# Kernel optimization log

Hardware: AMD Instinct MI355X
Metric: run time of the kernel (lower is better)

## Reference

```python
import jax, jax.numpy as jnp
import numpy as np

E = 8       # n_experts
TOPK = 2    # n_activated_experts


def setup_inputs() -> dict:
    key = jax.random.key(0)
    ks = jax.random.split(key, 5)
    B, T, C, F = 2, 1024, 1024, 2816
    scale = 0.02
    return {
        "x": jax.random.normal(ks[0], (B, T, C), dtype=jnp.float32),
        "Wg": jax.random.normal(ks[1], (C, E), dtype=jnp.float32) * scale,
        "W1": jax.random.normal(ks[2], (E, C, F), dtype=jnp.float32) * scale,
        "W3": jax.random.normal(ks[3], (E, C, F), dtype=jnp.float32) * scale,
        "W2": jax.random.normal(ks[4], (E, F, C), dtype=jnp.float32) * scale,
    }


def reference(x, Wg, W1, W3, W2):
    B, T, C = x.shape
    xt = x.reshape(-1, C)                                  # [N, C], N = B*T
    router = xt @ Wg                                       # [N, E]
    probs, indices = jax.lax.top_k(router, TOPK)           # [N, K] each, descending like torch.topk
    probs = jax.nn.softmax(probs.astype(jnp.float32), axis=1).astype(x.dtype)
    # combine[n, e] = sum_k probs[n, k] * (indices[n, k] == e)
    onehot = (indices[:, :, None] == jnp.arange(E)).astype(x.dtype)  # [N, K, E]
    combine = jnp.einsum("nk,nke->ne", probs, onehot)      # [N, E]
    # SwiGLU experts, computed densely then combined with routing weights
    h1 = jnp.einsum("nc,ecf->enf", xt, W1)                 # [E, N, F]
    h3 = jnp.einsum("nc,ecf->enf", xt, W3)                 # [E, N, F]
    h = jax.nn.silu(h1) * h3                               # [E, N, F]
    yexp = jnp.einsum("enf,efc->enc", h, W2)               # [E, N, C]
    y = jnp.einsum("ne,enc->nc", combine, yexp)            # [N, C]
    return (y.reshape(B, T, C), indices)
```

## Files before the change

kernel.cpp:

```cpp
#include <hip/hip_runtime.h>
#include <hip/hip_bf16.h>

#define NE 8
#define C 1024
#define F 2816

typedef __bf16 bf16_t;
typedef bf16_t bf16x8 __attribute__((ext_vector_type(8)));
typedef float f32x4 __attribute__((ext_vector_type(4)));

__device__ inline unsigned pk2(float a, float b) {
    union { bf16_t h[2]; unsigned u; } x;
    x.h[0] = (bf16_t)a; x.h[1] = (bf16_t)b;
    return x.u;
}

__device__ __forceinline__ void async_ld16(const bf16_t* g, bf16_t* l) {
    __builtin_amdgcn_global_load_lds(
        (const __attribute__((address_space(1))) unsigned int*)g,
        (__attribute__((address_space(3))) unsigned int*)l, 16, 0, 0);
}

__global__ void router_kernel(const float* __restrict__ x, const float* __restrict__ Wg,
                              float* __restrict__ probs, int* __restrict__ idxbuf,
                              float* __restrict__ out_idx, bf16_t* __restrict__ xb) {
    const int n = blockIdx.x;
    const int lane = threadIdx.x;
    const float* xr = x + (size_t)n * C;
    bf16_t* xbr = xb + (size_t)n * C;
    float acc[NE] = {0.f, 0.f, 0.f, 0.f, 0.f, 0.f, 0.f, 0.f};
    #pragma unroll
    for (int i = 0; i < C / 64; i++) {
        int c = i * 64 + lane;
        float xv = xr[c];
        xbr[c] = (bf16_t)xv;
        const float4* w = (const float4*)(Wg + (size_t)c * NE);
        float4 w0 = w[0], w1 = w[1];
        acc[0] += xv * w0.x; acc[1] += xv * w0.y; acc[2] += xv * w0.z; acc[3] += xv * w0.w;
        acc[4] += xv * w1.x; acc[5] += xv * w1.y; acc[6] += xv * w1.z; acc[7] += xv * w1.w;
    }
    #pragma unroll
    for (int off = 32; off >= 1; off >>= 1)
        #pragma unroll
        for (int e = 0; e < NE; e++) acc[e] += __shfl_down(acc[e], off);
    if (lane == 0) {
        float v0 = -1e30f, v1 = -1e30f; int i0 = 0, i1 = 0;
        #pragma unroll
        for (int e = 0; e < NE; e++) {
            float v = acc[e];
            if (v > v0)      { v1 = v0; i1 = i0; v0 = v; i0 = e; }
            else if (v > v1) { v1 = v; i1 = e; }
        }
        float e1 = __expf(v1 - v0);
        probs[n * 2]     = 1.0f / (1.0f + e1);
        probs[n * 2 + 1] = e1 / (1.0f + e1);
        idxbuf[n * 2]     = i0;
        idxbuf[n * 2 + 1] = i1;
        out_idx[n * 2]     = (float)i0;
        out_idx[n * 2 + 1] = (float)i1;
    }
}

__global__ void group_kernel(const int* __restrict__ idxbuf, int* __restrict__ rowinfo,
                             int* __restrict__ counts, int* __restrict__ offs, int N) {
    __shared__ int cnt[NE], run[NE], base[NE];
    const int t = threadIdx.x;
    if (t < NE) { cnt[t] = 0; run[t] = 0; }
    __syncthreads();
    for (int i = t; i < N * 2; i += blockDim.x) atomicAdd(&cnt[idxbuf[i]], 1);
    __syncthreads();
    if (t == 0) { int s = 0; for (int e = 0; e < NE; e++) { base[e] = s; s += cnt[e]; } }
    __syncthreads();
    for (int i = t; i < N * 2; i += blockDim.x) {
        int e = idxbuf[i];
        int p = atomicAdd(&run[e], 1);
        rowinfo[base[e] + p] = i;
    }
    if (t < NE) { counts[t] = cnt[t]; offs[t] = base[t]; }
}

__global__ __launch_bounds__(256)
void convert_kernel(const float* __restrict__ W1, const float* __restrict__ W3,
                    const float* __restrict__ W2, bf16_t* __restrict__ Wt1,
                    bf16_t* __restrict__ Wt3, bf16_t* __restrict__ Wt2) {
    const int yy = blockIdx.y;
    const int which = yy >> 3, e = yy & 7;
    const float* src; bf16_t* dst; int R, Cc;
    if (which == 0)      { src = W1; dst = Wt1; R = C; Cc = F; }
    else if (which == 1) { src = W3; dst = Wt3; R = C; Cc = F; }
    else                 { src = W2; dst = Wt2; R = F; Cc = C; }
    src += (size_t)e * C * F;
    dst += (size_t)e * C * F;
    const int tiles_r = R >> 6;
    const int bx = blockIdx.x;
    const int tr = bx % tiles_r, tc = bx / tiles_r;
    const int t = threadIdx.x;
    __shared__ __align__(16) bf16_t tile[64 * 72];

    const int mr = t >> 4, mc = t & 15;
    const float* sp = src + (size_t)(tr * 64 + mr * 4) * Cc + tc * 64 + mc * 4;
    float4 v0 = *(const float4*)(sp);
    float4 v1 = *(const float4*)(sp + Cc);
    float4 v2 = *(const float4*)(sp + 2 * (size_t)Cc);
    float4 v3 = *(const float4*)(sp + 3 * (size_t)Cc);
    uint2 u;
    u.x = pk2(v0.x, v1.x); u.y = pk2(v2.x, v3.x); *(uint2*)&tile[(mc * 4 + 0) * 72 + mr * 4] = u;
    u.x = pk2(v0.y, v1.y); u.y = pk2(v2.y, v3.y); *(uint2*)&tile[(mc * 4 + 1) * 72 + mr * 4] = u;
    u.x = pk2(v0.z, v1.z); u.y = pk2(v2.z, v3.z); *(uint2*)&tile[(mc * 4 + 2) * 72 + mr * 4] = u;
    u.x = pk2(v0.w, v1.w); u.y = pk2(v2.w, v3.w); *(uint2*)&tile[(mc * 4 + 3) * 72 + mr * 4] = u;
    __syncthreads();
    const int dc = t >> 2, rc = (t & 3) * 16;
    uint4 o0 = *(uint4*)&tile[dc * 72 + rc];
    uint4 o1 = *(uint4*)&tile[dc * 72 + rc + 8];
    bf16_t* dp = dst + (size_t)(tc * 64 + dc) * R + tr * 64 + rc;
    *(uint4*)(dp)     = o0;
    *(uint4*)(dp + 8) = o1;
}

__global__ __launch_bounds__(256, 2)
void gemm1_kernel(const bf16_t* __restrict__ xb, const bf16_t* __restrict__ Wt1,
                  const bf16_t* __restrict__ Wt3, const int* __restrict__ rowinfo,
                  const int* __restrict__ counts, const int* __restrict__ offs,
                  bf16_t* __restrict__ hbuf) {
    const int e = blockIdx.z;
    const int cnt = counts[e];
    const int m0 = blockIdx.y << 7;
    if (m0 >= cnt) return;
    const int base = offs[e];
    const int f0 = blockIdx.x << 7;
    const int t = threadIdx.x;
    const int lane = t & 63, w = t >> 6;
    const int lr = lane & 15, quad = lane >> 4;
    const int wm = (w >> 1) << 6, wn = (w & 1) << 6;

    __shared__ __align__(16) bf16_t As[128 * 32];
    __shared__ __align__(16) bf16_t B1s[128 * 32];
    __shared__ __align__(16) bf16_t B3s[128 * 32];

    const int srow = w * 16 + (lane >> 2);
    const int skoff = (lane & 3) * 8;
    const int r0 = min(m0 + srow, cnt - 1);
    const int r1 = min(m0 + 64 + srow, cnt - 1);
    const bf16_t* ag0 = xb + (size_t)(rowinfo[base + r0] >> 1) * C + skoff;
    const bf16_t* ag1 = xb + (size_t)(rowinfo[base + r1] >> 1) * C + skoff;
    const bf16_t* b1g0 = Wt1 + ((size_t)e * F + f0 + srow) * C + skoff;
    const bf16_t* b1g1 = b1g0 + (size_t)64 * C;
    const bf16_t* b3g0 = Wt3 + ((size_t)e * F + f0 + srow) * C + skoff;
    const bf16_t* b3g1 = b3g0 + (size_t)64 * C;
    bf16_t* lA0 = &As[(w * 16) * 32];
    bf16_t* lA1 = &As[(64 + w * 16) * 32];
    bf16_t* lB10 = &B1s[(w * 16) * 32];
    bf16_t* lB11 = &B1s[(64 + w * 16) * 32];
    bf16_t* lB30 = &B3s[(w * 16) * 32];
    bf16_t* lB31 = &B3s[(64 + w * 16) * 32];

    f32x4 acc1[4][4], acc3[4][4];
    const f32x4 zero = {0.f, 0.f, 0.f, 0.f};
    #pragma unroll
    for (int im = 0; im < 4; im++)
        #pragma unroll
        for (int in = 0; in < 4; in++) { acc1[im][in] = zero; acc3[im][in] = zero; }

    for (int kc = 0; kc < C; kc += 32) {
        async_ld16(ag0 + kc, lA0);
        async_ld16(ag1 + kc, lA1);
        async_ld16(b1g0 + kc, lB10);
        async_ld16(b1g1 + kc, lB11);
        async_ld16(b3g0 + kc, lB30);
        async_ld16(b3g1 + kc, lB31);
        __syncthreads();
        bf16x8 af[4], b1f[4], b3f[4];
        #pragma unroll
        for (int im = 0; im < 4; im++)
            af[im] = *(const bf16x8*)(&As[(wm + im * 16 + lr) * 32 + quad * 8]);
        #pragma unroll
        for (int in = 0; in < 4; in++) {
            b1f[in] = *(const bf16x8*)(&B1s[(wn + in * 16 + lr) * 32 + quad * 8]);
            b3f[in] = *(const bf16x8*)(&B3s[(wn + in * 16 + lr) * 32 + quad * 8]);
        }
        #pragma unroll
        for (int im = 0; im < 4; im++)
            #pragma unroll
            for (int in = 0; in < 4; in++) {
                acc1[im][in] = __builtin_amdgcn_mfma_f32_16x16x32_bf16(af[im], b1f[in], acc1[im][in], 0, 0, 0);
                acc3[im][in] = __builtin_amdgcn_mfma_f32_16x16x32_bf16(af[im], b3f[in], acc3[im][in], 0, 0, 0);
            }
        __syncthreads();
    }
    #pragma unroll
    for (int im = 0; im < 4; im++) {
        #pragma unroll
        for (int r = 0; r < 4; r++) {
            const int row = wm + im * 16 + quad * 4 + r;
            const int gi = m0 + row;
            if (gi < cnt) {
                bf16_t* hp = hbuf + (size_t)(base + gi) * F + f0 + wn + lr;
                #pragma unroll
                for (int in = 0; in < 4; in++) {
                    float h1 = acc1[im][in][r], h3 = acc3[im][in][r];
                    float s = h1 / (1.0f + __expf(-h1)) * h3;
                    hp[in * 16] = (bf16_t)s;
                }
            }
        }
    }
}

__global__ __launch_bounds__(256, 2)
void gemm2_kernel(const bf16_t* __restrict__ hbuf, const bf16_t* __restrict__ Wt2,
                  const int* __restrict__ rowinfo, const int* __restrict__ counts,
                  const int* __restrict__ offs, float* __restrict__ part,
                  int PK, int nslots) {
    const int z = blockIdx.z;
    const int e = z & 7, ks = z >> 3;
    const int cnt = counts[e];
    const int m0 = blockIdx.y << 7;
    if (m0 >= cnt) return;
    const int base = offs[e];
    const int c0 = blockIdx.x << 7;
    const int t = threadIdx.x;
    const int lane = t & 63, w = t >> 6;
    const int lr = lane & 15, quad = lane >> 4;
    const int wm = (w >> 1) << 6, wn = (w & 1) << 6;

    const int klen = F / PK;
    const int kbeg = ks * klen, kend = kbeg + klen;

    __shared__ __align__(16) bf16_t As[128 * 32];
    __shared__ __align__(16) bf16_t Bs[128 * 32];

    const int srow = w * 16 + (lane >> 2);
    const int skoff = (lane & 3) * 8;
    const int r0 = min(m0 + srow, cnt - 1);
    const int r1 = min(m0 + 64 + srow, cnt - 1);
    const bf16_t* ag0 = hbuf + (size_t)(base + r0) * F + skoff;
    const bf16_t* ag1 = hbuf + (size_t)(base + r1) * F + skoff;
    const bf16_t* bg0 = Wt2 + ((size_t)e * C + c0 + srow) * F + skoff;
    const bf16_t* bg1 = bg0 + (size_t)64 * F;
    bf16_t* lA0 = &As[(w * 16) * 32];
    bf16_t* lA1 = &As[(64 + w * 16) * 32];
    bf16_t* lB0 = &Bs[(w * 16) * 32];
    bf16_t* lB1 = &Bs[(64 + w * 16) * 32];

    f32x4 acc[4][4];
    const f32x4 zero = {0.f, 0.f, 0.f, 0.f};
    #pragma unroll
    for (int im = 0; im < 4; im++)
        #pragma unroll
        for (int in = 0; in < 4; in++) acc[im][in] = zero;

    for (int kc = kbeg; kc < kend; kc += 32) {
        async_ld16(ag0 + kc, lA0);
        async_ld16(ag1 + kc, lA1);
        async_ld16(bg0 + kc, lB0);
        async_ld16(bg1 + kc, lB1);
        __syncthreads();
        bf16x8 af[4], bf_[4];
        #pragma unroll
        for (int im = 0; im < 4; im++)
            af[im] = *(const bf16x8*)(&As[(wm + im * 16 + lr) * 32 + quad * 8]);
        #pragma unroll
        for (int in = 0; in < 4; in++)
            bf_[in] = *(const bf16x8*)(&Bs[(wn + in * 16 + lr) * 32 + quad * 8]);
        #pragma unroll
        for (int im = 0; im < 4; im++)
            #pragma unroll
            for (int in = 0; in < 4; in++)
                acc[im][in] = __builtin_amdgcn_mfma_f32_16x16x32_bf16(af[im], bf_[in], acc[im][in], 0, 0, 0);
        __syncthreads();
    }
    #pragma unroll
    for (int im = 0; im < 4; im++) {
        #pragma unroll
        for (int r = 0; r < 4; r++) {
            const int row = wm + im * 16 + quad * 4 + r;
            const int gi = m0 + row;
            if (gi < cnt) {
                const int slot = rowinfo[base + gi];
                float* cp = part + ((size_t)ks * nslots + slot) * C + c0 + wn + lr;
                #pragma unroll
                for (int in = 0; in < 4; in++) cp[in * 16] = acc[im][in][r];
            }
        }
    }
}

__global__ void reduce_kernel(const float* __restrict__ part, const float* __restrict__ probs,
                              float* __restrict__ y, int PK, int nslots) {
    const int idx = blockIdx.x * blockDim.x + threadIdx.x;
    const int n = idx >> 8;
    const int c = (idx & 255) * 4;
    const size_t ksstride = (size_t)nslots * C;
    const float* b0 = part + ((size_t)n * 2) * C + c;
    float4 s0 = {0.f, 0.f, 0.f, 0.f}, s1 = {0.f, 0.f, 0.f, 0.f};
    for (int ks = 0; ks < PK; ks++) {
        float4 a = *(const float4*)(b0 + ks * ksstride);
        float4 b = *(const float4*)(b0 + ks * ksstride + C);
        s0.x += a.x; s0.y += a.y; s0.z += a.z; s0.w += a.w;
        s1.x += b.x; s1.y += b.y; s1.z += b.z; s1.w += b.w;
    }
    const float p0 = probs[n * 2], p1 = probs[n * 2 + 1];
    float4 o;
    o.x = p0 * s0.x + p1 * s1.x;
    o.y = p0 * s0.y + p1 * s1.y;
    o.z = p0 * s0.z + p1 * s1.z;
    o.w = p0 * s0.w + p1 * s1.w;
    *(float4*)(y + (size_t)n * C + c) = o;
}

extern "C" void kernel_launch(void* const* d_in, const int* in_sizes, int n_in,
                              void* d_out, int out_size, void* d_ws, size_t ws_size,
                              hipStream_t stream) {
    const float* x  = (const float*)d_in[0];
    const float* Wg = (const float*)d_in[1];
    const float* W1 = (const float*)d_in[2];
    const float* W3 = (const float*)d_in[3];
    const float* W2 = (const float*)d_in[4];
    const int N = in_sizes[0] / C;
    const int nslots = N * 2;

    float* y = (float*)d_out;
    float* out_idx = y + (size_t)N * C;

    char* ws = (char*)d_ws;
    size_t off = 0;
    auto alloc = [&](size_t bytes) { size_t p = off; off = (off + bytes + 255) & ~(size_t)255; return p; };
    float* probs   = (float*)(ws + alloc((size_t)nslots * 4));
    int* idxbuf    = (int*)(ws + alloc((size_t)nslots * 4));
    int* rowinfo   = (int*)(ws + alloc((size_t)nslots * 4));
    int* counts    = (int*)(ws + alloc(64));
    int* offs      = (int*)(ws + alloc(64));
    bf16_t* xb     = (bf16_t*)(ws + alloc((size_t)N * C * 2));
    bf16_t* hbuf   = (bf16_t*)(ws + alloc((size_t)nslots * F * 2));
    bf16_t* Wt1    = (bf16_t*)(ws + alloc((size_t)NE * C * F * 2));
    bf16_t* Wt3    = (bf16_t*)(ws + alloc((size_t)NE * C * F * 2));
    bf16_t* Wt2    = (bf16_t*)(ws + alloc((size_t)NE * C * F * 2));
    const size_t partbytes = (size_t)nslots * C * 4;
    int PK = 1;
    if (off + 4 * partbytes + 1024 <= ws_size) PK = 4;
    else if (off + 2 * partbytes + 1024 <= ws_size) PK = 2;
    float* part = (float*)(ws + alloc((size_t)PK * partbytes));

    const int mtiles = nslots / 128;

    router_kernel<<<N, 64, 0, stream>>>(x, Wg, probs, idxbuf, out_idx, xb);
    group_kernel<<<1, 256, 0, stream>>>(idxbuf, rowinfo, counts, offs, N);
    convert_kernel<<<dim3(704, 24), 256, 0, stream>>>(W1, W3, W2, Wt1, Wt3, Wt2);
    gemm1_kernel<<<dim3(F / 128, mtiles, NE), 256, 0, stream>>>(xb, Wt1, Wt3, rowinfo, counts, offs, hbuf);
    gemm2_kernel<<<dim3(C / 128, mtiles, NE * PK), 256, 0, stream>>>(hbuf, Wt2, rowinfo, counts, offs, part, PK, nslots);
    reduce_kernel<<<(N * C / 4 + 255) / 256, 256, 0, stream>>>(part, probs, y, PK, nslots);
}
```

Measured before the change: 455.3 us.

## Transpose weights in registers without LDS and store split-K partials as bf16

The weight conversion kernel now has each thread load an 8x8 fp32 block and write eight transposed 16-byte bf16 rows directly. This removes the shared-memory tile and barrier and cuts the grid to 128x128 tiles. The split-K partial buffer written by gemm2 and read by the reduce kernel changes from fp32 to bf16, halving that traffic. The reduce kernel is widened to 8 elements per thread. The trade-offs are strided, less coalesced global reads and writes in the transpose, and added rounding error from bf16 partials.

```diff
diff --git a/kernel.cpp b/kernel.cpp
--- a/kernel.cpp
+++ b/kernel.cpp
@@ -91,30 +91,37 @@
     else                 { src = W2; dst = Wt2; R = F; Cc = C; }
     src += (size_t)e * C * F;
     dst += (size_t)e * C * F;
-    const int tiles_r = R >> 6;
-    const int bx = blockIdx.x;
-    const int tr = bx % tiles_r, tc = bx / tiles_r;
+    const int tiles_r = R >> 7;
+    const int trb = blockIdx.x % tiles_r, tcb = blockIdx.x / tiles_r;
     const int t = threadIdx.x;
-    __shared__ __align__(16) bf16_t tile[64 * 72];
-
-    const int mr = t >> 4, mc = t & 15;
-    const float* sp = src + (size_t)(tr * 64 + mr * 4) * Cc + tc * 64 + mc * 4;
-    float4 v0 = *(const float4*)(sp);
-    float4 v1 = *(const float4*)(sp + Cc);
-    float4 v2 = *(const float4*)(sp + 2 * (size_t)Cc);
-    float4 v3 = *(const float4*)(sp + 3 * (size_t)Cc);
-    uint2 u;
-    u.x = pk2(v0.x, v1.x); u.y = pk2(v2.x, v3.x); *(uint2*)&tile[(mc * 4 + 0) * 72 + mr * 4] = u;
-    u.x = pk2(v0.y, v1.y); u.y = pk2(v2.y, v3.y); *(uint2*)&tile[(mc * 4 + 1) * 72 + mr * 4] = u;
-    u.x = pk2(v0.z, v1.z); u.y = pk2(v2.z, v3.z); *(uint2*)&tile[(mc * 4 + 2) * 72 + mr * 4] = u;
-    u.x = pk2(v0.w, v1.w); u.y = pk2(v2.w, v3.w); *(uint2*)&tile[(mc * 4 + 3) * 72 + mr * 4] = u;
-    __syncthreads();
-    const int dc = t >> 2, rc = (t & 3) * 16;
-    uint4 o0 = *(uint4*)&tile[dc * 72 + rc];
-    uint4 o1 = *(uint4*)&tile[dc * 72 + rc + 8];
-    bf16_t* dp = dst + (size_t)(tc * 64 + dc) * R + tr * 64 + rc;
-    *(uint4*)(dp)     = o0;
-    *(uint4*)(dp + 8) = o1;
+    const int R0 = trb * 128 + (t >> 4) * 8;
+    const int C0 = tcb * 128 + (t & 15) * 8;
+
+    const float* sp = src + (size_t)R0 * Cc + C0;
+    float4 va[8], vb[8];
+    #pragma unroll
+    for (int i = 0; i < 8; i++) {
+        va[i] = *(const float4*)(sp + (size_t)i * Cc);
+        vb[i] = *(const float4*)(sp + (size_t)i * Cc + 4);
+    }
+    bf16_t* dp = dst + (size_t)C0 * R + R0;
+    uint4 o;
+    o.x = pk2(va[0].x, va[1].x); o.y = pk2(va[2].x, va[3].x); o.z = pk2(va[4].x, va[5].x); o.w = pk2(va[6].x, va[7].x);
+    *(uint4*)(dp + 0 * (size_t)R) = o;
+    o.x = pk2(va[0].y, va[1].y); o.y = pk2(va[2].y, va[3].y); o.z = pk2(va[4].y, va[5].y); o.w = pk2(va[6].y, va[7].y);
+    *(uint4*)(dp + 1 * (size_t)R) = o;
+    o.x = pk2(va[0].z, va[1].z); o.y = pk2(va[2].z, va[3].z); o.z = pk2(va[4].z, va[5].z); o.w = pk2(va[6].z, va[7].z);
+    *(uint4*)(dp + 2 * (size_t)R) = o;
+    o.x = pk2(va[0].w, va[1].w); o.y = pk2(va[2].w, va[3].w); o.z = pk2(va[4].w, va[5].w); o.w = pk2(va[6].w, va[7].w);
+    *(uint4*)(dp + 3 * (size_t)R) = o;
+    o.x = pk2(vb[0].x, vb[1].x); o.y = pk2(vb[2].x, vb[3].x); o.z = pk2(vb[4].x, vb[5].x); o.w = pk2(vb[6].x, vb[7].x);
+    *(uint4*)(dp + 4 * (size_t)R) = o;
+    o.x = pk2(vb[0].y, vb[1].y); o.y = pk2(vb[2].y, vb[3].y); o.z = pk2(vb[4].y, vb[5].y); o.w = pk2(vb[6].y, vb[7].y);
+    *(uint4*)(dp + 5 * (size_t)R) = o;
+    o.x = pk2(vb[0].z, vb[1].z); o.y = pk2(vb[2].z, vb[3].z); o.z = pk2(vb[4].z, vb[5].z); o.w = pk2(vb[6].z, vb[7].z);
+    *(uint4*)(dp + 6 * (size_t)R) = o;
+    o.x = pk2(vb[0].w, vb[1].w); o.y = pk2(vb[2].w, vb[3].w); o.z = pk2(vb[4].w, vb[5].w); o.w = pk2(vb[6].w, vb[7].w);
+    *(uint4*)(dp + 7 * (size_t)R) = o;
 }
 
 __global__ __launch_bounds__(256, 2)
@@ -209,7 +216,7 @@
 __global__ __launch_bounds__(256, 2)
 void gemm2_kernel(const bf16_t* __restrict__ hbuf, const bf16_t* __restrict__ Wt2,
                   const int* __restrict__ rowinfo, const int* __restrict__ counts,
-                  const int* __restrict__ offs, float* __restrict__ part,
+                  const int* __restrict__ offs, bf16_t* __restrict__ part,
                   int PK, int nslots) {
     const int z = blockIdx.z;
     const int e = z & 7, ks = z >> 3;
@@ -277,35 +284,40 @@
             const int gi = m0 + row;
             if (gi < cnt) {
                 const int slot = rowinfo[base + gi];
-                float* cp = part + ((size_t)ks * nslots + slot) * C + c0 + wn + lr;
+                bf16_t* cp = part + ((size_t)ks * nslots + slot) * C + c0 + wn + lr;
                 #pragma unroll
-                for (int in = 0; in < 4; in++) cp[in * 16] = acc[im][in][r];
+                for (int in = 0; in < 4; in++) cp[in * 16] = (bf16_t)acc[im][in][r];
             }
         }
     }
 }
 
-__global__ void reduce_kernel(const float* __restrict__ part, const float* __restrict__ probs,
+__global__ void reduce_kernel(const bf16_t* __restrict__ part, const float* __restrict__ probs,
                               float* __restrict__ y, int PK, int nslots) {
     const int idx = blockIdx.x * blockDim.x + threadIdx.x;
-    const int n = idx >> 8;
-    const int c = (idx & 255) * 4;
+    const int n = idx >> 7;
+    const int c = (idx & 127) * 8;
     const size_t ksstride = (size_t)nslots * C;
-    const float* b0 = part + ((size_t)n * 2) * C + c;
-    float4 s0 = {0.f, 0.f, 0.f, 0.f}, s1 = {0.f, 0.f, 0.f, 0.f};
+    const bf16_t* b0 = part + ((size_t)n * 2) * C + c;
+    float s0[8] = {0, 0, 0, 0, 0, 0, 0, 0}, s1[8] = {0, 0, 0, 0, 0, 0, 0, 0};
     for (int ks = 0; ks < PK; ks++) {
-        float4 a = *(const float4*)(b0 + ks * ksstride);
-        float4 b = *(const float4*)(b0 + ks * ksstride + C);
-        s0.x += a.x; s0.y += a.y; s0.z += a.z; s0.w += a.w;
-        s1.x += b.x; s1.y += b.y; s1.z += b.z; s1.w += b.w;
+        bf16x8 a = *(const bf16x8*)(b0 + ks * ksstride);
+        bf16x8 b = *(const bf16x8*)(b0 + ks * ksstride + C);
+        #pragma unroll
+        for (int i = 0; i < 8; i++) { s0[i] += (float)a[i]; s1[i] += (float)b[i]; }
     }
     const float p0 = probs[n * 2], p1 = probs[n * 2 + 1];
-    float4 o;
-    o.x = p0 * s0.x + p1 * s1.x;
-    o.y = p0 * s0.y + p1 * s1.y;
-    o.z = p0 * s0.z + p1 * s1.z;
-    o.w = p0 * s0.w + p1 * s1.w;
-    *(float4*)(y + (size_t)n * C + c) = o;
+    float4 o0, o1;
+    o0.x = p0 * s0[0] + p1 * s1[0];
+    o0.y = p0 * s0[1] + p1 * s1[1];
+    o0.z = p0 * s0[2] + p1 * s1[2];
+    o0.w = p0 * s0[3] + p1 * s1[3];
+    o1.x = p0 * s0[4] + p1 * s1[4];
+    o1.y = p0 * s0[5] + p1 * s1[5];
+    o1.z = p0 * s0[6] + p1 * s1[6];
+    o1.w = p0 * s0[7] + p1 * s1[7];
+    *(float4*)(y + (size_t)n * C + c) = o0;
+    *(float4*)(y + (size_t)n * C + c + 4) = o1;
 }
 
 extern "C" void kernel_launch(void* const* d_in, const int* in_sizes, int n_in,
@@ -335,18 +347,18 @@
     bf16_t* Wt1    = (bf16_t*)(ws + alloc((size_t)NE * C * F * 2));
     bf16_t* Wt3    = (bf16_t*)(ws + alloc((size_t)NE * C * F * 2));
     bf16_t* Wt2    = (bf16_t*)(ws + alloc((size_t)NE * C * F * 2));
-    const size_t partbytes = (size_t)nslots * C * 4;
+    const size_t partbytes = (size_t)nslots * C * 2;
     int PK = 1;
     if (off + 4 * partbytes + 1024 <= ws_size) PK = 4;
     else if (off + 2 * partbytes + 1024 <= ws_size) PK = 2;
-    float* part = (float*)(ws + alloc((size_t)PK * partbytes));
+    bf16_t* part = (bf16_t*)(ws + alloc((size_t)PK * partbytes));
 
     const int mtiles = nslots / 128;
 
     router_kernel<<<N, 64, 0, stream>>>(x, Wg, probs, idxbuf, out_idx, xb);
     group_kernel<<<1, 256, 0, stream>>>(idxbuf, rowinfo, counts, offs, N);
-    convert_kernel<<<dim3(704, 24), 256, 0, stream>>>(W1, W3, W2, Wt1, Wt3, Wt2);
+    convert_kernel<<<dim3(176, 24), 256, 0, stream>>>(W1, W3, W2, Wt1, Wt3, Wt2);
     gemm1_kernel<<<dim3(F / 128, mtiles, NE), 256, 0, stream>>>(xb, Wt1, Wt3, rowinfo, counts, offs, hbuf);
     gemm2_kernel<<<dim3(C / 128, mtiles, NE * PK), 256, 0, stream>>>(hbuf, Wt2, rowinfo, counts, offs, part, PK, nslots);
-    reduce_kernel<<<(N * C / 4 + 255) / 256, 256, 0, stream>>>(part, probs, y, PK, nslots);
-}
+    reduce_kernel<<<(N * C / 8 + 255) / 256, 256, 0, stream>>>(part, probs, y, PK, nslots);
+}
```

New measurement: 451.9 us. Within noise of the previous version (-0.7%).
